# Kernel optimization log

Hardware: AMD Instinct MI355X
Metric: run time of the kernel (lower is better)

The kernel has to match this reference:

```python
import jax, jax.numpy as jnp
import numpy as np

N_NODES = 100000
N_EDGES = 800000
D = 64
N_ITERS = 3  # n_layers - 1


def setup_inputs() -> dict:
    key = jax.random.key(0)
    k1, k2, k3, k4 = jax.random.split(key, 4)
    x = jax.random.normal(k1, (N_NODES, D), dtype=jnp.float32)
    edge_index = jax.random.randint(k2, (2, N_EDGES), 0, N_NODES, dtype=jnp.int64)
    edge_weight = jax.random.uniform(k3, (N_EDGES,), dtype=jnp.float32)
    # Linear(64, 64) weight, scaled ~ kaiming so 3 stacked layers stay bounded
    W = jax.random.normal(k4, (D, D), dtype=jnp.float32) * (1.0 / np.sqrt(D))
    b = jnp.zeros((D,), dtype=jnp.float32)
    return {"x": x, "edge_index": edge_index, "edge_weight": edge_weight, "W": W, "b": b}


def reference(x, edge_index, edge_weight, W, b):
    # Faithful math of RPINetEncoder.forward: (n_layers-1) iterations of
    # LinearAggregation (weighted scatter-add message passing + shared Linear)
    # followed by ReLU. Dropout output is discarded in the original -> no-op.
    src = edge_index[0]
    dst = edge_index[1]
    n = x.shape[0]
    for _ in range(N_ITERS):
        msgs = edge_weight[:, None] * x[src]                      # [E, D] gather
        agg = jax.ops.segment_sum(msgs, dst, num_segments=n)      # [N, D] scatter-add
        x = jax.nn.relu(agg @ W.T + b)                            # shared linear + relu
    return x
```

## Files before the change

### kernel.cpp

```cpp
#include <hip/hip_runtime.h>
#include <hip/hip_bf16.h>

#define D 64
#define FP_SCALE 262144.0f
#define FP_INV   (1.0f / 262144.0f)
#define NPC 64
#define ASTR 68

__device__ __forceinline__ unsigned short f2bf(float f) {
    unsigned int u = __float_as_uint(f);
    u += 0x7fffu + ((u >> 16) & 1u);
    return (unsigned short)(u >> 16);
}

__global__ void hist_kernel(const int* __restrict__ dst, int* __restrict__ counts, int E) {
    int e = blockIdx.x * blockDim.x + threadIdx.x;
    if (e < E) atomicAdd(&counts[dst[e]], 1);
}

__global__ void part_kernel(const int* __restrict__ counts, int* __restrict__ partial, int N) {
    __shared__ int ws4[4];
    int t = threadIdx.x, lane = t & 63, w = t >> 6;
    int n = blockIdx.x * 256 + t;
    int c = (n < N) ? counts[n] : 0;
    #pragma unroll
    for (int off = 32; off > 0; off >>= 1) c += __shfl_down(c, off);
    if (lane == 0) ws4[w] = c;
    __syncthreads();
    if (t == 0) partial[blockIdx.x] = ws4[0] + ws4[1] + ws4[2] + ws4[3];
}

__global__ void scan_kernel(int* __restrict__ partial, int nb) {
    __shared__ int wsum[8];
    int t = threadIdx.x, lane = t & 63, w = t >> 6;
    int carry = 0;
    for (int base = 0; base < nb; base += 512) {
        int i = base + t;
        int v = (i < nb) ? partial[i] : 0;
        int incl = v;
        #pragma unroll
        for (int off = 1; off < 64; off <<= 1) {
            int x = __shfl_up(incl, off);
            if (lane >= off) incl += x;
        }
        if (lane == 63) wsum[w] = incl;
        __syncthreads();
        int wpre = 0;
        for (int j = 0; j < w; ++j) wpre += wsum[j];
        int tot = 0;
        for (int j = 0; j < 8; ++j) tot += wsum[j];
        if (i < nb) partial[i] = carry + wpre + incl - v;
        carry += tot;
        __syncthreads();
    }
}

__global__ void seg_kernel(const int* __restrict__ counts, const int* __restrict__ partial,
                           int* __restrict__ cursor, int* __restrict__ blockStart, int N) {
    __shared__ int ws4[4];
    int t = threadIdx.x, lane = t & 63, w = t >> 6;
    int n = blockIdx.x * 256 + t;
    int c = (n < N) ? counts[n] : 0;
    int incl = c;
    #pragma unroll
    for (int off = 1; off < 64; off <<= 1) {
        int x = __shfl_up(incl, off);
        if (lane >= off) incl += x;
    }
    if (lane == 63) ws4[w] = incl;
    __syncthreads();
    int wpre = 0;
    for (int j = 0; j < w; ++j) wpre += ws4[j];
    int st = partial[blockIdx.x] + wpre + incl - c;
    if (n < N) {
        cursor[n] = st;
        if ((n & (NPC - 1)) == 0) blockStart[n / NPC] = st;
    }
}

__global__ void fill_kernel(const int* __restrict__ src, const int* __restrict__ dst,
                            const float* __restrict__ ew, int* __restrict__ cursor,
                            unsigned long long* __restrict__ perm64, int E) {
    int e = blockIdx.x * blockDim.x + threadIdx.x;
    if (e < E) {
        int d = dst[e];
        int p = atomicAdd(&cursor[d], 1);
        unsigned lo = ((unsigned)src[e] << 6) | (unsigned)(d & (NPC - 1));
        perm64[p] = ((unsigned long long)__float_as_uint(ew[e] * FP_SCALE) << 32) | lo;
    }
}

__global__ void cvt_kernel(const float* __restrict__ in, unsigned short* __restrict__ out, int n4) {
    int i = blockIdx.x * blockDim.x + threadIdx.x;
    if (i >= n4) return;
    float4 v = reinterpret_cast<const float4*>(in)[i];
    ushort4 o;
    o.x = f2bf(v.x); o.y = f2bf(v.y); o.z = f2bf(v.z); o.w = f2bf(v.w);
    reinterpret_cast<ushort4*>(out)[i] = o;
}

template<bool OUT_BF>
__global__ void agg_fused_kernel(const unsigned short* __restrict__ xb,
                                 const unsigned long long* __restrict__ perm64,
                                 const int* __restrict__ blockStart,
                                 const float* __restrict__ W,
                                 const float* __restrict__ bias,
                                 void* __restrict__ xout,
                                 int N, int E) {
    __shared__ int acc[NPC * ASTR];
    __shared__ float Wt[D][D];
    __shared__ float bsh[D];
    int t = threadIdx.x;
    int bid = blockIdx.x;
    int nodeBase = bid * NPC;
    int nodeEnd = min(nodeBase + NPC, N);
    int es = blockStart[bid];
    int ee = (bid + 1 < (int)gridDim.x) ? blockStart[bid + 1] : E;

    for (int i = t; i < NPC * ASTR / 4; i += 256)
        reinterpret_cast<int4*>(acc)[i] = make_int4(0, 0, 0, 0);
    for (int i = t; i < D * D; i += 256) {
        int j = i >> 6, d = i & 63;
        Wt[d][j] = W[i] * FP_INV;
    }
    if (t < D) bsh[t] = bias[t];
    __syncthreads();

    int g = t >> 4;
    int c = (t & 15) << 2;
    for (int e = es + g; e < ee; e += 16) {
        unsigned long long pk = perm64[e];
        unsigned lo = (unsigned)pk;
        float w = __uint_as_float((unsigned)(pk >> 32));
        int slot = (int)(lo & (NPC - 1));
        int s = (int)(lo >> 6);
        uint2 u = *reinterpret_cast<const uint2*>(&xb[(size_t)s * D + c]);
        int base = slot * ASTR + c;
        atomicAdd(&acc[base + 0], (int)(w * __uint_as_float(u.x << 16)));
        atomicAdd(&acc[base + 1], (int)(w * __uint_as_float(u.x & 0xffff0000u)));
        atomicAdd(&acc[base + 2], (int)(w * __uint_as_float(u.y << 16)));
        atomicAdd(&acc[base + 3], (int)(w * __uint_as_float(u.y & 0xffff0000u)));
    }
    __syncthreads();

    int wave = t >> 6, lane = t & 63;
    int sBase = wave * 16;
    float o[16];
    #pragma unroll
    for (int i = 0; i < 16; ++i) o[i] = 0.f;
    for (int f = 0; f < D; f += 4) {
        float w0 = Wt[f + 0][lane];
        float w1 = Wt[f + 1][lane];
        float w2 = Wt[f + 2][lane];
        float w3 = Wt[f + 3][lane];
        #pragma unroll
        for (int i = 0; i < 16; ++i) {
            int4 ai = *reinterpret_cast<const int4*>(&acc[(sBase + i) * ASTR + f]);
            o[i] = fmaf((float)ai.x, w0,
                   fmaf((float)ai.y, w1,
                   fmaf((float)ai.z, w2,
                   fmaf((float)ai.w, w3, o[i]))));
        }
    }
    #pragma unroll
    for (int i = 0; i < 16; ++i) {
        int node = nodeBase + sBase + i;
        if (node < nodeEnd) {
            float v = fmaxf(bsh[lane] + o[i], 0.0f);
            size_t off = (size_t)node * D + lane;
            if (OUT_BF) ((unsigned short*)xout)[off] = f2bf(v);
            else        ((float*)xout)[off] = v;
        }
    }
}

__global__ void rpi_scatter_kernel(const float* __restrict__ x,
                                   const int* __restrict__ src,
                                   const int* __restrict__ dst,
                                   const float* __restrict__ ew,
                                   int* __restrict__ agg, int E) {
    int tid = blockIdx.x * blockDim.x + threadIdx.x;
    int e = tid >> 4;
    if (e >= E) return;
    int c = (tid & 15) << 2;
    int s = src[e], d = dst[e];
    float w = ew[e] * FP_SCALE;
    float4 v = *reinterpret_cast<const float4*>(&x[(size_t)s * D + c]);
    int* o = &agg[(size_t)d * D + c];
    atomicAdd(o + 0, (int)(w * v.x));
    atomicAdd(o + 1, (int)(w * v.y));
    atomicAdd(o + 2, (int)(w * v.z));
    atomicAdd(o + 3, (int)(w * v.w));
}

__global__ void rpi_linear_relu_kernel(const int* __restrict__ agg,
                                       const float* __restrict__ W,
                                       const float* __restrict__ b,
                                       float* __restrict__ out, int N) {
    __shared__ float Ws[D][D + 1];
    __shared__ float bs[D];
    int t = threadIdx.x;
    for (int i = t; i < D * D; i += 256) Ws[i >> 6][i & 63] = W[i];
    if (t < D) bs[t] = b[t];
    __syncthreads();
    int wave = t >> 6, lane = t & 63;
    int nwaves = gridDim.x * 4;
    for (int n = blockIdx.x * 4 + wave; n < N; n += nwaves) {
        const int* arow = &agg[(size_t)n * D];
        float acc = bs[lane];
        #pragma unroll
        for (int d = 0; d < D; ++d) acc = fmaf((float)arow[d] * FP_INV, Ws[lane][d], acc);
        out[(size_t)n * D + lane] = fmaxf(acc, 0.0f);
    }
}

extern "C" void kernel_launch(void* const* d_in, const int* in_sizes, int n_in,
                              void* d_out, int out_size, void* d_ws, size_t ws_size,
                              hipStream_t stream) {
    const float* x0 = (const float*)d_in[0];
    const int*   ei = (const int*)d_in[1];
    const float* ew = (const float*)d_in[2];
    const float* W  = (const float*)d_in[3];
    const float* b  = (const float*)d_in[4];
    float* out = (float*)d_out;

    int N = in_sizes[0] / D;
    int E = in_sizes[2];
    const int* src = ei;
    const int* dst = ei + E;

    int nb   = (N + 255) / 256;
    int nblk = (N + NPC - 1) / NPC;
    size_t xeb = (size_t)N * D * sizeof(unsigned short);
    size_t off = 0;
    size_t o_xb1  = off; off += xeb;
    size_t o_xb2  = off; off += xeb;
    size_t o_p64  = off; off += (size_t)E * sizeof(unsigned long long);
    size_t o_cnt  = off; off += (size_t)N * sizeof(int);
    size_t o_part = off; off += ((size_t)nb + 16) * sizeof(int);
    size_t o_bs   = off; off += ((size_t)nblk + 2) * sizeof(int);
    size_t need = off;

    if (ws_size >= need) {
        unsigned short* xb1 = (unsigned short*)((char*)d_ws + o_xb1);
        unsigned short* xb2 = (unsigned short*)((char*)d_ws + o_xb2);
        unsigned long long* perm64 = (unsigned long long*)((char*)d_ws + o_p64);
        int* cnt_cur    = (int*)((char*)d_ws + o_cnt);
        int* partial    = (int*)((char*)d_ws + o_part);
        int* blockStart = (int*)((char*)d_ws + o_bs);

        int eb = (E + 255) / 256;
        int n4 = N * D / 4;

        hipMemsetAsync(cnt_cur, 0, (size_t)N * sizeof(int), stream);
        hist_kernel<<<eb, 256, 0, stream>>>(dst, cnt_cur, E);
        part_kernel<<<nb, 256, 0, stream>>>(cnt_cur, partial, N);
        scan_kernel<<<1, 512, 0, stream>>>(partial, nb);
        seg_kernel <<<nb, 256, 0, stream>>>(cnt_cur, partial, cnt_cur, blockStart, N);
        fill_kernel<<<eb, 256, 0, stream>>>(src, dst, ew, cnt_cur, perm64, E);
        cvt_kernel <<<(n4 + 255) / 256, 256, 0, stream>>>(x0, xb1, n4);

        agg_fused_kernel<true> <<<nblk, 256, 0, stream>>>(xb1, perm64, blockStart, W, b, xb2, N, E);
        agg_fused_kernel<true> <<<nblk, 256, 0, stream>>>(xb2, perm64, blockStart, W, b, xb1, N, E);
        agg_fused_kernel<false><<<nblk, 256, 0, stream>>>(xb1, perm64, blockStart, W, b, out, N, E);
    } else {
        int* agg = (int*)d_ws;
        const float* xcur = x0;
        int sb = (E * 16 + 255) / 256;
        for (int it = 0; it < 3; ++it) {
            hipMemsetAsync(agg, 0, (size_t)N * D * sizeof(int), stream);
            rpi_scatter_kernel<<<sb, 256, 0, stream>>>(xcur, src, dst, ew, agg, E);
            rpi_linear_relu_kernel<<<2048, 256, 0, stream>>>(agg, W, b, out, N);
            xcur = out;
        }
    }
}
```

Measured before the change: 328.0 us.

## Permute LDS accumulator layout to avoid bank conflicts and unroll edge loop

Changes the shared-memory accumulator row stride from 68 to 65 and interleaves feature columns so each of the 16 lanes in an edge group hits a distinct bank, instead of four consecutive columns per lane. The edge loop is also unrolled to load four packed edge records per thread per iteration, raising memory-level parallelism before the LDS atomics. The matmul phase reads the accumulator as scalars under the new permuted layout instead of int4 vectors, which may cost more LDS instructions there.

New measurement: 313.7 us. -4.4%, faster.

```diff
diff --git a/kernel.cpp b/kernel.cpp
--- a/kernel.cpp
+++ b/kernel.cpp
@@ -5,7 +5,7 @@
 #define FP_SCALE 262144.0f
 #define FP_INV   (1.0f / 262144.0f)
 #define NPC 64
-#define ASTR 68
+#define ASTR 65
 
 __device__ __forceinline__ unsigned short f2bf(float f) {
     unsigned int u = __float_as_uint(f);
@@ -127,20 +127,40 @@
     __syncthreads();
 
     int g = t >> 4;
-    int c = (t & 15) << 2;
-    for (int e = es + g; e < ee; e += 16) {
+    int i16 = t & 15;
+    int gl = g & 3;
+    int w4 = g >> 2;
+
+#define EDGE_ATOMIC(pk)                                                         \
+    {                                                                           \
+        unsigned lo_ = (unsigned)(pk);                                          \
+        float w_ = __uint_as_float((unsigned)((pk) >> 32));                     \
+        int slot_ = (int)(lo_ & (NPC - 1));                                     \
+        int s_ = (int)(lo_ >> 6);                                               \
+        uint2 u_ = *reinterpret_cast<const uint2*>(&xb[(size_t)s_ * D + (i16 << 2)]); \
+        int base_ = slot_ * ASTR + i16;                                         \
+        atomicAdd(&acc[base_ +  0], (int)(w_ * __uint_as_float(u_.x << 16)));   \
+        atomicAdd(&acc[base_ + 16], (int)(w_ * __uint_as_float(u_.x & 0xffff0000u))); \
+        atomicAdd(&acc[base_ + 32], (int)(w_ * __uint_as_float(u_.y << 16)));   \
+        atomicAdd(&acc[base_ + 48], (int)(w_ * __uint_as_float(u_.y & 0xffff0000u))); \
+    }
+
+    int myOff = es + gl * 16 + w4 * 4;
+    int cnt = ee - es;
+    int kmax = cnt >> 6;
+    for (int k = 0; k < kmax; ++k) {
+        int e0 = myOff + (k << 6);
+        unsigned long long pk0 = perm64[e0 + 0];
+        unsigned long long pk1 = perm64[e0 + 1];
+        unsigned long long pk2 = perm64[e0 + 2];
+        unsigned long long pk3 = perm64[e0 + 3];
+        EDGE_ATOMIC(pk0); EDGE_ATOMIC(pk1); EDGE_ATOMIC(pk2); EDGE_ATOMIC(pk3);
+    }
+    for (int e = es + (kmax << 6) + g; e < ee; e += 16) {
         unsigned long long pk = perm64[e];
-        unsigned lo = (unsigned)pk;
-        float w = __uint_as_float((unsigned)(pk >> 32));
-        int slot = (int)(lo & (NPC - 1));
-        int s = (int)(lo >> 6);
-        uint2 u = *reinterpret_cast<const uint2*>(&xb[(size_t)s * D + c]);
-        int base = slot * ASTR + c;
-        atomicAdd(&acc[base + 0], (int)(w * __uint_as_float(u.x << 16)));
-        atomicAdd(&acc[base + 1], (int)(w * __uint_as_float(u.x & 0xffff0000u)));
-        atomicAdd(&acc[base + 2], (int)(w * __uint_as_float(u.y << 16)));
-        atomicAdd(&acc[base + 3], (int)(w * __uint_as_float(u.y & 0xffff0000u)));
-    }
+        EDGE_ATOMIC(pk);
+    }
+#undef EDGE_ATOMIC
     __syncthreads();
 
     int wave = t >> 6, lane = t & 63;
@@ -148,18 +168,19 @@
     float o[16];
     #pragma unroll
     for (int i = 0; i < 16; ++i) o[i] = 0.f;
-    for (int f = 0; f < D; f += 4) {
-        float w0 = Wt[f + 0][lane];
-        float w1 = Wt[f + 1][lane];
-        float w2 = Wt[f + 2][lane];
-        float w3 = Wt[f + 3][lane];
+    for (int q = 0; q < 16; ++q) {
+        float w0 = Wt[4 * q + 0][lane];
+        float w1 = Wt[4 * q + 1][lane];
+        float w2 = Wt[4 * q + 2][lane];
+        float w3 = Wt[4 * q + 3][lane];
         #pragma unroll
         for (int i = 0; i < 16; ++i) {
-            int4 ai = *reinterpret_cast<const int4*>(&acc[(sBase + i) * ASTR + f]);
-            o[i] = fmaf((float)ai.x, w0,
-                   fmaf((float)ai.y, w1,
-                   fmaf((float)ai.z, w2,
-                   fmaf((float)ai.w, w3, o[i]))));
+            int base = (sBase + i) * ASTR + q;
+            float a0 = (float)acc[base +  0];
+            float a1 = (float)acc[base + 16];
+            float a2 = (float)acc[base + 32];
+            float a3 = (float)acc[base + 48];
+            o[i] = fmaf(a0, w0, fmaf(a1, w1, fmaf(a2, w2, fmaf(a3, w3, o[i]))));
         }
     }
     #pragma unroll
```
